# Performance work log

Hardware: AMD Instinct MI355X
Metric: run time of the kernel (lower is better)

Reference implementation:

```python
import jax, jax.numpy as jnp
import numpy as np

HEADS = 16
NU = 1
EPS = 1e-6


def dpfp(k):
    """Deterministic Parameter-Free Projection, normalized. k: [..., d_k] -> [..., 2*d_k*NU]."""
    x = jax.nn.relu(jnp.concatenate([k, -k], axis=-1))  # [..., 2*d_k]
    x_rolled = jnp.concatenate([jnp.roll(x, i, axis=-1) for i in range(1, NU + 1)], axis=-1)
    x_repeat = jnp.concatenate([x] * NU, axis=-1)
    phi = x_repeat * x_rolled
    return phi / (jnp.sum(phi, axis=-1, keepdims=True) + EPS)


def setup_inputs() -> dict:
    key = jax.random.key(0)
    ks = jax.random.split(key, 7)
    S, B, D, H = 4096, 4, 1024, HEADS
    scale = 0.02
    return {
        "x": jax.random.normal(ks[0], (S, B, D), dtype=jnp.float32),
        "Wq": jax.random.normal(ks[1], (D, D), dtype=jnp.float32) * scale,
        "Wk": jax.random.normal(ks[2], (D, D), dtype=jnp.float32) * scale,
        "Wv": jax.random.normal(ks[3], (D, D), dtype=jnp.float32) * scale,
        "Wb": jax.random.normal(ks[4], (D, H), dtype=jnp.float32) * scale,
        "Wo": jax.random.normal(ks[5], (D, D), dtype=jnp.float32) * scale,
        "bo": jnp.zeros((D,), dtype=jnp.float32),
    }


def reference(x, Wq, Wk, Wv, Wb, Wo, bo):
    S, B, D = x.shape
    H = HEADS
    dk = D // H
    d_dot = 2 * dk * NU

    # Projections: [S, B, H, d_k] (bias-free linears + head split)
    q = dpfp((x @ Wq).reshape(S, B, H, dk))   # [S, B, H, d_dot]
    k = dpfp((x @ Wk).reshape(S, B, H, dk))   # [S, B, H, d_dot]
    v = (x @ Wv).reshape(S, B, H, dk)          # [S, B, H, d_k]
    beta = jax.nn.sigmoid(x @ Wb).reshape(S, B, H, 1)  # [S, B, H, 1]

    W0 = jnp.zeros((B, H, dk, d_dot), dtype=x.dtype)  # fast-weight state

    def step(W, inputs):
        k_i, v_i, q_i, b_i = inputs  # [B,H,d_dot], [B,H,dk], [B,H,d_dot], [B,H,1]
        v_bar = jnp.einsum('bhvk,bhk->bhv', W, k_i)
        W = W + jnp.einsum('bhv,bhk->bhvk', b_i * (v_i - v_bar), k_i)
        y = jnp.einsum('bhvk,bhk->bhv', W, q_i)  # [B, H, dk]
        return W, y.reshape(B, H * dk)

    _, outputs = jax.lax.scan(step, W0, (k, v, q, beta))  # [S, B, D]
    return outputs @ Wo + bo
```

## Files before the change

kernel.cpp:

```cpp
#include <hip/hip_runtime.h>

#define S_LEN 4096
#define BATCH 4
#define NROWS 16384
#define DIM   1024
#define CHUNK 32
#define NCHUNK (S_LEN / CHUNK)

typedef __attribute__((ext_vector_type(8))) short short8;
typedef __attribute__((ext_vector_type(4))) float floatx4;
typedef _Float16 half_t;
typedef __attribute__((ext_vector_type(8))) _Float16 half8;

__device__ __forceinline__ float bf2f(short s) {
    union { unsigned int u; float f; } c;
    c.u = ((unsigned int)(unsigned short)s) << 16;
    return c.f;
}
__device__ __forceinline__ short f2bf(float f) {
    union { float f; unsigned int u; } c; c.f = f;
    unsigned int r = c.u + 0x7fffu + ((c.u >> 16) & 1u);
    return (short)(r >> 16);
}
__device__ __forceinline__ void split_bf16(float x, short& hi, short& lo) {
    short h = f2bf(x);
    hi = h;
    lo = f2bf(x - bf2f(h));
}

__device__ __forceinline__ float row16_allreduce(float x) {
    union fi { float f; int i; };
    fi a, b;
    a.f = x;
    b.i = __builtin_amdgcn_update_dpp(0, a.i, 0xB1,  0xF, 0xF, true); a.f += b.f;
    b.i = __builtin_amdgcn_update_dpp(0, a.i, 0x4E,  0xF, 0xF, true); a.f += b.f;
    b.i = __builtin_amdgcn_update_dpp(0, a.i, 0x124, 0xF, 0xF, true); a.f += b.f;
    b.i = __builtin_amdgcn_update_dpp(0, a.i, 0x128, 0xF, 0xF, true); a.f += b.f;
    return a.f;
}

__global__ __launch_bounds__(256) void transpose_k(const float* __restrict__ W,
                                                   float* __restrict__ Wt,
                                                   int K, int N) {
    int idx = blockIdx.x * 256 + threadIdx.x;
    if (idx >= N * K) return;
    int n = idx / K;
    int k = idx - n * K;
    Wt[idx] = W[k * N + n];
}

template <typename AT, int MODE>
__global__ __launch_bounds__(256) void gemm_bt(const AT* __restrict__ A,
                                               const float* __restrict__ Bt,
                                               void* __restrict__ Cout,
                                               const float* __restrict__ bias,
                                               int N, int K) {
    __shared__ __align__(16) short As_h[64][40], As_l[64][40];
    __shared__ __align__(16) short Bs_h[64][40], Bs_l[64][40];
    const int tid  = threadIdx.x;
    const int wave = tid >> 6, lane = tid & 63;
    const int row0 = blockIdx.x * 64, col0 = blockIdx.y * 64;
    const int lr = tid >> 2, lc = (tid & 3) * 8;
    const AT*    Ap = A  + (size_t)(row0 + lr) * K + lc;
    const float* Bp = Bt + (size_t)(col0 + lr) * K + lc;
    const int am = wave * 16 + (lane & 15);
    const int ak = (lane >> 4) * 8;
    floatx4 acc[4];
    #pragma unroll
    for (int t = 0; t < 4; ++t) acc[t] = (floatx4){0.f, 0.f, 0.f, 0.f};

    for (int k0 = 0; k0 < K; k0 += 32) {
        float av[8], bv[8];
        if constexpr (sizeof(AT) == 4) {
            floatx4 a0 = *(const floatx4*)(Ap + k0);
            floatx4 a1 = *(const floatx4*)(Ap + k0 + 4);
            #pragma unroll
            for (int j = 0; j < 4; ++j) { av[j] = a0[j]; av[4 + j] = a1[j]; }
        } else {
            half8 a = *(const half8*)(Ap + k0);
            #pragma unroll
            for (int j = 0; j < 8; ++j) av[j] = (float)a[j];
        }
        floatx4 b0 = *(const floatx4*)(Bp + k0);
        floatx4 b1 = *(const floatx4*)(Bp + k0 + 4);
        #pragma unroll
        for (int j = 0; j < 4; ++j) { bv[j] = b0[j]; bv[4 + j] = b1[j]; }

        short8 ah, al, bh, bl;
        #pragma unroll
        for (int j = 0; j < 8; ++j) {
            short h, l;
            split_bf16(av[j], h, l); ah[j] = h; al[j] = l;
            split_bf16(bv[j], h, l); bh[j] = h; bl[j] = l;
        }
        *(short8*)&As_h[lr][lc] = ah;
        *(short8*)&As_l[lr][lc] = al;
        *(short8*)&Bs_h[lr][lc] = bh;
        *(short8*)&Bs_l[lr][lc] = bl;
        __syncthreads();
        short8 afh = *(const short8*)&As_h[am][ak];
        short8 afl = *(const short8*)&As_l[am][ak];
        #pragma unroll
        for (int t = 0; t < 4; ++t) {
            short8 bfh = *(const short8*)&Bs_h[t * 16 + (lane & 15)][ak];
            short8 bfl = *(const short8*)&Bs_l[t * 16 + (lane & 15)][ak];
            acc[t] = __builtin_amdgcn_mfma_f32_16x16x32_bf16(afh, bfh, acc[t], 0, 0, 0);
            acc[t] = __builtin_amdgcn_mfma_f32_16x16x32_bf16(afh, bfl, acc[t], 0, 0, 0);
            acc[t] = __builtin_amdgcn_mfma_f32_16x16x32_bf16(afl, bfh, acc[t], 0, 0, 0);
        }
        __syncthreads();
    }
    const int crow = row0 + wave * 16 + (lane >> 4) * 4;
    const int ccol = lane & 15;
    #pragma unroll
    for (int t = 0; t < 4; ++t) {
        int col = col0 + t * 16 + ccol;
        #pragma unroll
        for (int r = 0; r < 4; ++r) {
            int row = crow + r;
            float v = acc[t][r];
            if (MODE == 0) {
                float b = bias ? bias[col] : 0.f;
                ((float*)Cout)[(size_t)row * N + col] = v + b;
            } else {
                ((half_t*)Cout)[(size_t)row * 2048 + (col >> 6) * 128 + (col & 63)] = (half_t)v;
            }
        }
    }
}

__global__ __launch_bounds__(256) void beta_kernel(const float* __restrict__ X,
                                                   const float* __restrict__ Wbt,
                                                   float* __restrict__ Beta) {
    int wid  = (blockIdx.x * 256 + threadIdx.x) >> 6;
    int lane = threadIdx.x & 63;
    if (wid >= NROWS) return;
    const float* xr = X + (size_t)wid * DIM + lane * 16;
    float xv[16];
    #pragma unroll
    for (int j = 0; j < 4; ++j) {
        floatx4 v = *(const floatx4*)(xr + j * 4);
        #pragma unroll
        for (int e = 0; e < 4; ++e) xv[j * 4 + e] = v[e];
    }
    #pragma unroll 1
    for (int h = 0; h < 16; ++h) {
        const float* wr = Wbt + h * DIM + lane * 16;
        float s = 0.f;
        #pragma unroll
        for (int j = 0; j < 4; ++j) {
            floatx4 v = *(const floatx4*)(wr + j * 4);
            #pragma unroll
            for (int e = 0; e < 4; ++e) s = fmaf(xv[j * 4 + e], v[e], s);
        }
        #pragma unroll
        for (int off = 32; off; off >>= 1) s += __shfl_xor(s, off);
        if (lane == 0) Beta[wid * 16 + h] = 1.f / (1.f + __expf(-s));
    }
}

__global__ __launch_bounds__(256) void dpfp_h(half_t* __restrict__ P) {
    int gw   = (blockIdx.x * 256 + threadIdx.x) >> 6;
    int lane = threadIdx.x & 63;
    half_t* base = P + (size_t)gw * 128;
    float p  = (float)base[lane];
    float pm = __shfl(p, (lane + 63) & 63);
    float rp  = fmaxf(p, 0.f),  rn  = fmaxf(-p, 0.f);
    float rpm = fmaxf(pm, 0.f), rnm = fmaxf(-pm, 0.f);
    float aprev = (lane == 0) ? rnm : rpm;
    float bprev = (lane == 0) ? rpm : rnm;
    float phi_a = rp * aprev;
    float phi_b = rn * bprev;
    float s = phi_a + phi_b;
    #pragma unroll
    for (int off = 32; off; off >>= 1) s += __shfl_xor(s, off);
    float inv = 1.f / (s + 1e-6f);
    base[lane]      = (half_t)(phi_a * inv);
    base[64 + lane] = (half_t)(phi_b * inv);
}

__global__ __launch_bounds__(256, 1) void scan_kernel(const half_t* __restrict__ PhiK,
                                                      const half_t* __restrict__ PhiQ,
                                                      const float* __restrict__ V,
                                                      const float* __restrict__ Beta,
                                                      half_t* __restrict__ Y) {
    __shared__ float Ks[2][CHUNK][128];
    __shared__ float Qs[2][CHUNK][128];
    __shared__ float Vs[2][CHUNK][16];
    __shared__ float Bs[2][CHUNK];

    const int bh = blockIdx.x >> 2;
    const int rc = blockIdx.x & 3;
    const int b = bh >> 4, h = bh & 15;
    const int tid = threadIdx.x;
    const int row_l = tid >> 4;
    const int tc = tid & 15;
    const int vrow = rc * 16 + row_l;

    const half_t* kg = PhiK + h * 128;
    const half_t* qg = PhiQ + h * 128;
    const float*  vg = V + h * 64 + rc * 16;
    const float*  bg = Beta + h;
    half_t* ybase = Y + h * 64 + vrow;

    {
        #pragma unroll
        for (int rpt = 0; rpt < 2; ++rpt) {
            int i = rpt * 256 + tid;
            int st = i >> 4, seg = i & 15, row = i & 15;
            size_t r = (size_t)(st * BATCH + b);
            half8 kv = *(const half8*)(kg + r * 2048 + seg * 8);
            half8 qv = *(const half8*)(qg + r * 2048 + seg * 8);
            floatx4 klo, khi, qlo, qhi;
            #pragma unroll
            for (int j = 0; j < 4; ++j) {
                klo[j] = (float)kv[j]; khi[j] = (float)kv[4 + j];
                qlo[j] = (float)qv[j]; qhi[j] = (float)qv[4 + j];
            }
            *(floatx4*)&Ks[0][st][seg * 8]     = klo;
            *(floatx4*)&Ks[0][st][seg * 8 + 4] = khi;
            *(floatx4*)&Qs[0][st][seg * 8]     = qlo;
            *(floatx4*)&Qs[0][st][seg * 8 + 4] = qhi;
            Vs[0][st][row] = vg[r * 1024 + row];
        }
        if (tid < CHUNK) {
            size_t r = (size_t)(tid * BATCH + b);
            Bs[0][tid] = bg[r * 16];
        }
    }
    __syncthreads();

    float w[8];
    #pragma unroll
    for (int j = 0; j < 8; ++j) w[j] = 0.f;

    for (int c = 0; c < NCHUNK; ++c) {
        const int bufi = c & 1;
        const bool more = (c + 1 < NCHUNK);
        half8 pk[2], pq[2];
        float pv[2], pb = 0.f;
        if (more) {
            #pragma unroll
            for (int rpt = 0; rpt < 2; ++rpt) {
                int i = rpt * 256 + tid;
                int st = i >> 4, seg = i & 15, row = i & 15;
                size_t r = (size_t)(((c + 1) * CHUNK + st) * BATCH + b);
                pk[rpt] = *(const half8*)(kg + r * 2048 + seg * 8);
                pq[rpt] = *(const half8*)(qg + r * 2048 + seg * 8);
                pv[rpt] = vg[r * 1024 + row];
            }
            if (tid < CHUNK) {
                size_t r = (size_t)(((c + 1) * CHUNK + tid) * BATCH + b);
                pb = bg[r * 16];
            }
        }
        float Ak[8], Aq[8], Av, Ab;
        float Bk[8], Bq[8], Bv, Bb;
        {
            floatx4 k0 = *(const floatx4*)&Ks[bufi][0][tc * 8];
            floatx4 k1 = *(const floatx4*)&Ks[bufi][0][tc * 8 + 4];
            floatx4 q0 = *(const floatx4*)&Qs[bufi][0][tc * 8];
            floatx4 q1 = *(const floatx4*)&Qs[bufi][0][tc * 8 + 4];
            #pragma unroll
            for (int j = 0; j < 4; ++j) {
                Ak[j] = k0[j]; Ak[4 + j] = k1[j];
                Aq[j] = q0[j]; Aq[4 + j] = q1[j];
            }
            Av = Vs[bufi][0][row_l];
            Ab = Bs[bufi][0];
        }
        #pragma unroll 1
        for (int u = 0; u < CHUNK; u += 2) {
            {
                floatx4 k0 = *(const floatx4*)&Ks[bufi][u + 1][tc * 8];
                floatx4 k1 = *(const floatx4*)&Ks[bufi][u + 1][tc * 8 + 4];
                floatx4 q0 = *(const floatx4*)&Qs[bufi][u + 1][tc * 8];
                floatx4 q1 = *(const floatx4*)&Qs[bufi][u + 1][tc * 8 + 4];
                #pragma unroll
                for (int j = 0; j < 4; ++j) {
                    Bk[j] = k0[j]; Bk[4 + j] = k1[j];
                    Bq[j] = q0[j]; Bq[4 + j] = q1[j];
                }
                Bv = Vs[bufi][u + 1][row_l];
                Bb = Bs[bufi][u + 1];
            }
            {
                float d0 = w[0] * Ak[0], d1 = w[1] * Ak[1];
                d0 = fmaf(w[2], Ak[2], d0); d1 = fmaf(w[3], Ak[3], d1);
                d0 = fmaf(w[4], Ak[4], d0); d1 = fmaf(w[5], Ak[5], d1);
                d0 = fmaf(w[6], Ak[6], d0); d1 = fmaf(w[7], Ak[7], d1);
                float d = row16_allreduce(d0 + d1);
                float coef = Ab * (Av - d);
                #pragma unroll
                for (int j = 0; j < 8; ++j) w[j] = fmaf(coef, Ak[j], w[j]);
                float y0 = w[0] * Aq[0], y1 = w[1] * Aq[1];
                y0 = fmaf(w[2], Aq[2], y0); y1 = fmaf(w[3], Aq[3], y1);
                y0 = fmaf(w[4], Aq[4], y0); y1 = fmaf(w[5], Aq[5], y1);
                y0 = fmaf(w[6], Aq[6], y0); y1 = fmaf(w[7], Aq[7], y1);
                float y = row16_allreduce(y0 + y1);
                if (tc == 0)
                    ybase[(size_t)((c * CHUNK + u) * BATCH + b) * 1024] = (half_t)y;
            }
            if (u + 2 < CHUNK) {
                floatx4 k0 = *(const floatx4*)&Ks[bufi][u + 2][tc * 8];
                floatx4 k1 = *(const floatx4*)&Ks[bufi][u + 2][tc * 8 + 4];
                floatx4 q0 = *(const floatx4*)&Qs[bufi][u + 2][tc * 8];
                floatx4 q1 = *(const floatx4*)&Qs[bufi][u + 2][tc * 8 + 4];
                #pragma unroll
                for (int j = 0; j < 4; ++j) {
                    Ak[j] = k0[j]; Ak[4 + j] = k1[j];
                    Aq[j] = q0[j]; Aq[4 + j] = q1[j];
                }
                Av = Vs[bufi][u + 2][row_l];
                Ab = Bs[bufi][u + 2];
            }
            {
                float d0 = w[0] * Bk[0], d1 = w[1] * Bk[1];
                d0 = fmaf(w[2], Bk[2], d0); d1 = fmaf(w[3], Bk[3], d1);
                d0 = fmaf(w[4], Bk[4], d0); d1 = fmaf(w[5], Bk[5], d1);
                d0 = fmaf(w[6], Bk[6], d0); d1 = fmaf(w[7], Bk[7], d1);
                float d = row16_allreduce(d0 + d1);
                float coef = Bb * (Bv - d);
                #pragma unroll
                for (int j = 0; j < 8; ++j) w[j] = fmaf(coef, Bk[j], w[j]);
                float y0 = w[0] * Bq[0], y1 = w[1] * Bq[1];
                y0 = fmaf(w[2], Bq[2], y0); y1 = fmaf(w[3], Bq[3], y1);
                y0 = fmaf(w[4], Bq[4], y0); y1 = fmaf(w[5], Bq[5], y1);
                y0 = fmaf(w[6], Bq[6], y0); y1 = fmaf(w[7], Bq[7], y1);
                float y = row16_allreduce(y0 + y1);
                if (tc == 0)
                    ybase[(size_t)((c * CHUNK + u + 1) * BATCH + b) * 1024] = (half_t)y;
            }
        }
        if (more) {
            const int bufn = bufi ^ 1;
            #pragma unroll
            for (int rpt = 0; rpt < 2; ++rpt) {
                int i = rpt * 256 + tid;
                int st = i >> 4, seg = i & 15, row = i & 15;
                floatx4 klo, khi, qlo, qhi;
                #pragma unroll
                for (int j = 0; j < 4; ++j) {
                    klo[j] = (float)pk[rpt][j]; khi[j] = (float)pk[rpt][4 + j];
                    qlo[j] = (float)pq[rpt][j]; qhi[j] = (float)pq[rpt][4 + j];
                }
                *(floatx4*)&Ks[bufn][st][seg * 8]     = klo;
                *(floatx4*)&Ks[bufn][st][seg * 8 + 4] = khi;
                *(floatx4*)&Qs[bufn][st][seg * 8]     = qlo;
                *(floatx4*)&Qs[bufn][st][seg * 8 + 4] = qhi;
                Vs[bufn][st][row] = pv[rpt];
            }
            if (tid < CHUNK) Bs[bufn][tid] = pb;
        }
        __syncthreads();
    }
}

extern "C" void kernel_launch(void* const* d_in, const int* in_sizes, int n_in,
                              void* d_out, int out_size, void* d_ws, size_t ws_size,
                              hipStream_t stream) {
    const float* x  = (const float*)d_in[0];
    const float* Wq = (const float*)d_in[1];
    const float* Wk = (const float*)d_in[2];
    const float* Wv = (const float*)d_in[3];
    const float* Wb = (const float*)d_in[4];
    const float* Wo = (const float*)d_in[5];
    const float* bo = (const float*)d_in[6];

    char* ws = (char*)d_ws;
    size_t off = 0;
    auto alloc = [&](size_t bytes) -> void* {
        void* p = ws + off;
        off += (bytes + 255) & ~(size_t)255;
        return p;
    };
    half_t* PhiQ = (half_t*)alloc((size_t)NROWS * 2048 * 2);
    half_t* PhiK = (half_t*)alloc((size_t)NROWS * 2048 * 2);
    half_t* Yb   = (half_t*)alloc((size_t)NROWS * 1024 * 2);
    float*  Beta = (float*)alloc((size_t)NROWS * 16 * 4);
    float*  Wqt  = (float*)alloc((size_t)1024 * 1024 * 4);
    float*  Wkt  = (float*)alloc((size_t)1024 * 1024 * 4);
    float*  Wvt  = (float*)alloc((size_t)1024 * 1024 * 4);
    float*  Wot  = (float*)alloc((size_t)1024 * 1024 * 4);
    float*  Wbt  = (float*)alloc((size_t)16 * 1024 * 4);
    float*  Vb   = (float*)d_out;

    transpose_k<<<4096, 256, 0, stream>>>(Wq, Wqt, 1024, 1024);
    transpose_k<<<4096, 256, 0, stream>>>(Wk, Wkt, 1024, 1024);
    transpose_k<<<4096, 256, 0, stream>>>(Wv, Wvt, 1024, 1024);
    transpose_k<<<4096, 256, 0, stream>>>(Wo, Wot, 1024, 1024);
    transpose_k<<<64,   256, 0, stream>>>(Wb, Wbt, 1024, 16);

    dim3 ggrid(NROWS / 64, DIM / 64);
    const int dgrid = (NROWS * 16) / 4;
    gemm_bt<float, 1><<<ggrid, 256, 0, stream>>>(x, Wqt, PhiQ, nullptr, DIM, DIM);
    dpfp_h<<<dgrid, 256, 0, stream>>>(PhiQ);
    gemm_bt<float, 1><<<ggrid, 256, 0, stream>>>(x, Wkt, PhiK, nullptr, DIM, DIM);
    dpfp_h<<<dgrid, 256, 0, stream>>>(PhiK);
    gemm_bt<float, 0><<<ggrid, 256, 0, stream>>>(x, Wvt, Vb, nullptr, DIM, DIM);
    beta_kernel<<<NROWS / 4, 256, 0, stream>>>(x, Wbt, Beta);
    scan_kernel<<<256, 256, 0, stream>>>(PhiK, PhiQ, Vb, Beta, Yb);
    gemm_bt<half_t, 0><<<ggrid, 256, 0, stream>>>(Yb, Wot, d_out, bo, DIM, DIM);
}
```

Measured before the change: 1.720 ms.

## Split scan work across twice as many blocks with 32-lane row reductions

The fast-weight scan is repartitioned so that each block owns 8 value rows instead of 16, and each row is spread over 32 lanes holding 4 state columns instead of 16 lanes holding 8. The grid doubles to 512 blocks, with launch bounds allowing two blocks per CU, and a ds_swizzle step extends the row reduction to 32 lanes. This shortens the per-thread serial dependency chain and uses more CUs for the latency-bound recurrence. The cost is a longer reduction per step and K/Q chunk loads duplicated across twice as many blocks.

```diff
diff --git a/kernel.cpp b/kernel.cpp
--- a/kernel.cpp
+++ b/kernel.cpp
@@ -37,6 +37,15 @@
     b.i = __builtin_amdgcn_update_dpp(0, a.i, 0x124, 0xF, 0xF, true); a.f += b.f;
     b.i = __builtin_amdgcn_update_dpp(0, a.i, 0x128, 0xF, 0xF, true); a.f += b.f;
     return a.f;
+}
+
+__device__ __forceinline__ float row32_allreduce(float x) {
+    x = row16_allreduce(x);
+    union fi { float f; int i; };
+    fi a, b;
+    a.f = x;
+    b.i = __builtin_amdgcn_ds_swizzle(a.i, 0x401F);
+    return a.f + b.f;
 }
 
 __global__ __launch_bounds__(256) void transpose_k(const float* __restrict__ W,
@@ -179,27 +188,27 @@
     base[64 + lane] = (half_t)(phi_b * inv);
 }
 
-__global__ __launch_bounds__(256, 1) void scan_kernel(const half_t* __restrict__ PhiK,
+__global__ __launch_bounds__(256, 2) void scan_kernel(const half_t* __restrict__ PhiK,
                                                       const half_t* __restrict__ PhiQ,
                                                       const float* __restrict__ V,
                                                       const float* __restrict__ Beta,
                                                       half_t* __restrict__ Y) {
     __shared__ float Ks[2][CHUNK][128];
     __shared__ float Qs[2][CHUNK][128];
-    __shared__ float Vs[2][CHUNK][16];
+    __shared__ float Vs[2][CHUNK][8];
     __shared__ float Bs[2][CHUNK];
 
-    const int bh = blockIdx.x >> 2;
-    const int rc = blockIdx.x & 3;
+    const int bh = blockIdx.x & 63;
+    const int rc = blockIdx.x >> 6;
     const int b = bh >> 4, h = bh & 15;
     const int tid = threadIdx.x;
-    const int row_l = tid >> 4;
-    const int tc = tid & 15;
-    const int vrow = rc * 16 + row_l;
+    const int row_l = tid >> 5;
+    const int tc = tid & 31;
+    const int vrow = rc * 8 + row_l;
 
     const half_t* kg = PhiK + h * 128;
     const half_t* qg = PhiQ + h * 128;
-    const float*  vg = V + h * 64 + rc * 16;
+    const float*  vg = V + h * 64 + rc * 8;
     const float*  bg = Beta + h;
     half_t* ybase = Y + h * 64 + vrow;
 
@@ -207,7 +216,7 @@
         #pragma unroll
         for (int rpt = 0; rpt < 2; ++rpt) {
             int i = rpt * 256 + tid;
-            int st = i >> 4, seg = i & 15, row = i & 15;
+            int st = i >> 4, seg = i & 15;
             size_t r = (size_t)(st * BATCH + b);
             half8 kv = *(const half8*)(kg + r * 2048 + seg * 8);
             half8 qv = *(const half8*)(qg + r * 2048 + seg * 8);
@@ -221,6 +230,10 @@
             *(floatx4*)&Ks[0][st][seg * 8 + 4] = khi;
             *(floatx4*)&Qs[0][st][seg * 8]     = qlo;
             *(floatx4*)&Qs[0][st][seg * 8 + 4] = qhi;
+        }
+        {
+            int st = tid >> 3, row = tid & 7;
+            size_t r = (size_t)(st * BATCH + b);
             Vs[0][st][row] = vg[r * 1024 + row];
         }
         if (tid < CHUNK) {
@@ -230,104 +243,85 @@
     }
     __syncthreads();
 
-    float w[8];
+    float w[4];
     #pragma unroll
-    for (int j = 0; j < 8; ++j) w[j] = 0.f;
+    for (int j = 0; j < 4; ++j) w[j] = 0.f;
 
     for (int c = 0; c < NCHUNK; ++c) {
         const int bufi = c & 1;
         const bool more = (c + 1 < NCHUNK);
         half8 pk[2], pq[2];
-        float pv[2], pb = 0.f;
+        float pv = 0.f, pb = 0.f;
         if (more) {
             #pragma unroll
             for (int rpt = 0; rpt < 2; ++rpt) {
                 int i = rpt * 256 + tid;
-                int st = i >> 4, seg = i & 15, row = i & 15;
+                int st = i >> 4, seg = i & 15;
                 size_t r = (size_t)(((c + 1) * CHUNK + st) * BATCH + b);
                 pk[rpt] = *(const half8*)(kg + r * 2048 + seg * 8);
                 pq[rpt] = *(const half8*)(qg + r * 2048 + seg * 8);
-                pv[rpt] = vg[r * 1024 + row];
+            }
+            {
+                int st = tid >> 3, row = tid & 7;
+                size_t r = (size_t)(((c + 1) * CHUNK + st) * BATCH + b);
+                pv = vg[r * 1024 + row];
             }
             if (tid < CHUNK) {
                 size_t r = (size_t)(((c + 1) * CHUNK + tid) * BATCH + b);
                 pb = bg[r * 16];
             }
         }
-        float Ak[8], Aq[8], Av, Ab;
-        float Bk[8], Bq[8], Bv, Bb;
+        float Ak[4], Aq[4], Av, Ab;
+        float Bk[4], Bq[4], Bv, Bb;
         {
-            floatx4 k0 = *(const floatx4*)&Ks[bufi][0][tc * 8];
-            floatx4 k1 = *(const floatx4*)&Ks[bufi][0][tc * 8 + 4];
-            floatx4 q0 = *(const floatx4*)&Qs[bufi][0][tc * 8];
-            floatx4 q1 = *(const floatx4*)&Qs[bufi][0][tc * 8 + 4];
-            #pragma unroll
-            for (int j = 0; j < 4; ++j) {
-                Ak[j] = k0[j]; Ak[4 + j] = k1[j];
-                Aq[j] = q0[j]; Aq[4 + j] = q1[j];
-            }
+            floatx4 k0 = *(const floatx4*)&Ks[bufi][0][tc * 4];
+            floatx4 q0 = *(const floatx4*)&Qs[bufi][0][tc * 4];
+            #pragma unroll
+            for (int j = 0; j < 4; ++j) { Ak[j] = k0[j]; Aq[j] = q0[j]; }
             Av = Vs[bufi][0][row_l];
             Ab = Bs[bufi][0];
         }
         #pragma unroll 1
         for (int u = 0; u < CHUNK; u += 2) {
             {
-                floatx4 k0 = *(const floatx4*)&Ks[bufi][u + 1][tc * 8];
-                floatx4 k1 = *(const floatx4*)&Ks[bufi][u + 1][tc * 8 + 4];
-                floatx4 q0 = *(const floatx4*)&Qs[bufi][u + 1][tc * 8];
-                floatx4 q1 = *(const floatx4*)&Qs[bufi][u + 1][tc * 8 + 4];
+                floatx4 k0 = *(const floatx4*)&Ks[bufi][u + 1][tc * 4];
+                floatx4 q0 = *(const floatx4*)&Qs[bufi][u + 1][tc * 4];
                 #pragma unroll
-                for (int j = 0; j < 4; ++j) {
-                    Bk[j] = k0[j]; Bk[4 + j] = k1[j];
-                    Bq[j] = q0[j]; Bq[4 + j] = q1[j];
-                }
+                for (int j = 0; j < 4; ++j) { Bk[j] = k0[j]; Bq[j] = q0[j]; }
                 Bv = Vs[bufi][u + 1][row_l];
                 Bb = Bs[bufi][u + 1];
             }
             {
                 float d0 = w[0] * Ak[0], d1 = w[1] * Ak[1];
                 d0 = fmaf(w[2], Ak[2], d0); d1 = fmaf(w[3], Ak[3], d1);
-                d0 = fmaf(w[4], Ak[4], d0); d1 = fmaf(w[5], Ak[5], d1);
-                d0 = fmaf(w[6], Ak[6], d0); d1 = fmaf(w[7], Ak[7], d1);
-                float d = row16_allreduce(d0 + d1);
+                float d = row32_allreduce(d0 + d1);
                 float coef = Ab * (Av - d);
                 #pragma unroll
-                for (int j = 0; j < 8; ++j) w[j] = fmaf(coef, Ak[j], w[j]);
+                for (int j = 0; j < 4; ++j) w[j] = fmaf(coef, Ak[j], w[j]);
                 float y0 = w[0] * Aq[0], y1 = w[1] * Aq[1];
                 y0 = fmaf(w[2], Aq[2], y0); y1 = fmaf(w[3], Aq[3], y1);
-                y0 = fmaf(w[4], Aq[4], y0); y1 = fmaf(w[5], Aq[5], y1);
-                y0 = fmaf(w[6], Aq[6], y0); y1 = fmaf(w[7], Aq[7], y1);
-                float y = row16_allreduce(y0 + y1);
+                float y = row32_allreduce(y0 + y1);
                 if (tc == 0)
                     ybase[(size_t)((c * CHUNK + u) * BATCH + b) * 1024] = (half_t)y;
             }
             if (u + 2 < CHUNK) {
-                floatx4 k0 = *(const floatx4*)&Ks[bufi][u + 2][tc * 8];
-                floatx4 k1 = *(const floatx4*)&Ks[bufi][u + 2][tc * 8 + 4];
-                floatx4 q0 = *(const floatx4*)&Qs[bufi][u + 2][tc * 8];
-                floatx4 q1 = *(const floatx4*)&Qs[bufi][u + 2][tc * 8 + 4];
+                floatx4 k0 = *(const floatx4*)&Ks[bufi][u + 2][tc * 4];
+                floatx4 q0 = *(const floatx4*)&Qs[bufi][u + 2][tc * 4];
                 #pragma unroll
-                for (int j = 0; j < 4; ++j) {
-                    Ak[j] = k0[j]; Ak[4 + j] = k1[j];
-                    Aq[j] = q0[j]; Aq[4 + j] = q1[j];
-                }
+                for (int j = 0; j < 4; ++j) { Ak[j] = k0[j]; Aq[j] = q0[j]; }
                 Av = Vs[bufi][u + 2][row_l];
                 Ab = Bs[bufi][u + 2];
             }
             {
                 float d0 = w[0] * Bk[0], d1 = w[1] * Bk[1];
                 d0 = fmaf(w[2], Bk[2], d0); d1 = fmaf(w[3], Bk[3], d1);
-                d0 = fmaf(w[4], Bk[4], d0); d1 = fmaf(w[5], Bk[5], d1);
-                d0 = fmaf(w[6], Bk[6], d0); d1 = fmaf(w[7], Bk[7], d1);
-                float d = row16_allreduce(d0 + d1);
+                float d = row32_allreduce(d0 + d1);
                 float coef = Bb * (Bv - d);
                 #pragma unroll
-                for (int j = 0; j < 8; ++j) w[j] = fmaf(coef, Bk[j], w[j]);
+                for (int j = 0; j < 4; ++j) w[j] = fmaf(coef, Bk[j], w[j]);
                 float y0 = w[0] * Bq[0], y1 = w[1] * Bq[1];
                 y0 = fmaf(w[2], Bq[2], y0); y1 = fmaf(w[3], Bq[3], y1);
-                y0 = fmaf(w[4], Bq[4], y0); y1 = fmaf(w[5], Bq[5], y1);
-                y0 = fmaf(w[6], Bq[6], y0); y1 = fmaf(w[7], Bq[7], y1);
-                float y = row16_allreduce(y0 + y1);
+                float y = row32_allreduce(y0 + y1);
                 if (tc == 0)
                     ybase[(size_t)((c * CHUNK + u + 1) * BATCH + b) * 1024] = (half_t)y;
             }
@@ -337,7 +331,7 @@
             #pragma unroll
             for (int rpt = 0; rpt < 2; ++rpt) {
                 int i = rpt * 256 + tid;
-                int st = i >> 4, seg = i & 15, row = i & 15;
+                int st = i >> 4, seg = i & 15;
                 floatx4 klo, khi, qlo, qhi;
                 #pragma unroll
                 for (int j = 0; j < 4; ++j) {
@@ -348,7 +342,10 @@
                 *(floatx4*)&Ks[bufn][st][seg * 8 + 4] = khi;
                 *(floatx4*)&Qs[bufn][st][seg * 8]     = qlo;
                 *(floatx4*)&Qs[bufn][st][seg * 8 + 4] = qhi;
-                Vs[bufn][st][row] = pv[rpt];
+            }
+            {
+                int st = tid >> 3, row = tid & 7;
+                Vs[bufn][st][row] = pv;
             }
             if (tid < CHUNK) Bs[bufn][tid] = pb;
         }
@@ -399,6 +396,6 @@
     dpfp_h<<<dgrid, 256, 0, stream>>>(PhiK);
     gemm_bt<float, 0><<<ggrid, 256, 0, stream>>>(x, Wvt, Vb, nullptr, DIM, DIM);
     beta_kernel<<<NROWS / 4, 256, 0, stream>>>(x, Wbt, Beta);
-    scan_kernel<<<256, 256, 0, stream>>>(PhiK, PhiQ, Vb, Beta, Yb);
+    scan_kernel<<<512, 256, 0, stream>>>(PhiK, PhiQ, Vb, Beta, Yb);
     gemm_bt<half_t, 0><<<ggrid, 256, 0, stream>>>(Yb, Wot, d_out, bo, DIM, DIM);
 }
```

New measurement: 1.777 ms. 3.3% more time.

## Process delta-rule scan two steps at a time using precomputed Gram terms

Applied to the files above, without the earlier changes.

The scan now advances two timesteps per pair. For each pair it precomputes the k_even·k_odd, k_even·q_even, k_even·q_odd and k_odd·q_odd inner products into shared memory at the start of each chunk. All four dot products against the old state are then issued together and corrected algebraically with these Gram terms. This breaks the serial dependency between consecutive steps' reductions, so four independent allreduces can overlap instead of four serialized ones. The cost is an extra Gram pass and a barrier per chunk, more registers for the double-buffered operands, and a different floating-point summation order.

```diff
diff --git a/kernel.cpp b/kernel.cpp
--- a/kernel.cpp
+++ b/kernel.cpp
@@ -179,6 +179,58 @@
     base[64 + lane] = (half_t)(phi_b * inv);
 }
 
+
+#define LOADSTEP(DK, DQ, STEP)                                              \
+    {                                                                       \
+        floatx4 _ka = *(const floatx4*)&Ks[bufi][STEP][tc * 8];             \
+        floatx4 _kb = *(const floatx4*)&Ks[bufi][STEP][tc * 8 + 4];         \
+        floatx4 _qa = *(const floatx4*)&Qs[bufi][STEP][tc * 8];             \
+        floatx4 _qb = *(const floatx4*)&Qs[bufi][STEP][tc * 8 + 4];         \
+        for (int _i = 0; _i < 4; ++_i) {                                    \
+            DK[_i] = _ka[_i]; DK[4 + _i] = _kb[_i];                         \
+            DQ[_i] = _qa[_i]; DQ[4 + _i] = _qb[_i];                         \
+        }                                                                   \
+    }
+
+#define DOT8(RES, X, Y)                                                     \
+    {                                                                       \
+        float _s0 = X[0] * Y[0], _s1 = X[1] * Y[1];                         \
+        _s0 = fmaf(X[2], Y[2], _s0); _s1 = fmaf(X[3], Y[3], _s1);           \
+        _s0 = fmaf(X[4], Y[4], _s0); _s1 = fmaf(X[5], Y[5], _s1);           \
+        _s0 = fmaf(X[6], Y[6], _s0); _s1 = fmaf(X[7], Y[7], _s1);           \
+        RES = _s0 + _s1;                                                    \
+    }
+
+#define PAIR(CEK, CEQ, COK, COQ, CEV, CEB, COV, COB, CG,                    \
+             NEK, NEQ, NOK, NOQ, NEV, NEB, NOV, NOB, NG, P)                 \
+    {                                                                       \
+        if ((P) + 1 < 16) {                                                 \
+            LOADSTEP(NEK, NEQ, 2 * (P) + 2);                                \
+            LOADSTEP(NOK, NOQ, 2 * (P) + 3);                                \
+            NEV = Vs[bufi][2 * (P) + 2][row_l];                             \
+            NEB = Bs[bufi][2 * (P) + 2];                                    \
+            NOV = Vs[bufi][2 * (P) + 3][row_l];                             \
+            NOB = Bs[bufi][2 * (P) + 3];                                    \
+            NG  = *(const floatx4*)&GramLDS[(P) + 1][0];                    \
+        }                                                                   \
+        float _e0, _e1, _f0, _f1;                                           \
+        DOT8(_e0, w, CEK); DOT8(_e1, w, COK);                               \
+        DOT8(_f0, w, CEQ); DOT8(_f1, w, COQ);                               \
+        _e0 = row16_allreduce(_e0); _e1 = row16_allreduce(_e1);             \
+        _f0 = row16_allreduce(_f0); _f1 = row16_allreduce(_f1);             \
+        float _c0 = CEB * (CEV - _e0);                                      \
+        float _d1 = fmaf(_c0, CG[0], _e1);                                  \
+        float _c1 = COB * (COV - _d1);                                      \
+        float _y0 = fmaf(_c0, CG[1], _f0);                                  \
+        float _y1 = fmaf(_c1, CG[3], fmaf(_c0, CG[2], _f1));                \
+        for (int _j = 0; _j < 8; ++_j)                                      \
+            w[_j] = fmaf(_c1, COK[_j], fmaf(_c0, CEK[_j], w[_j]));          \
+        if (tc == 0) {                                                      \
+            ybase[(size_t)((cc * CHUNK + 2 * (P))     * BATCH + b) * 1024] = (half_t)_y0; \
+            ybase[(size_t)((cc * CHUNK + 2 * (P) + 1) * BATCH + b) * 1024] = (half_t)_y1; \
+        }                                                                   \
+    }
+
 __global__ __launch_bounds__(256, 1) void scan_kernel(const half_t* __restrict__ PhiK,
                                                       const half_t* __restrict__ PhiQ,
                                                       const float* __restrict__ V,
@@ -188,6 +240,7 @@
     __shared__ float Qs[2][CHUNK][128];
     __shared__ float Vs[2][CHUNK][16];
     __shared__ float Bs[2][CHUNK];
+    __shared__ float GramLDS[16][4];
 
     const int bh = blockIdx.x >> 2;
     const int rc = blockIdx.x & 3;
@@ -234,9 +287,32 @@
     #pragma unroll
     for (int j = 0; j < 8; ++j) w[j] = 0.f;
 
-    for (int c = 0; c < NCHUNK; ++c) {
-        const int bufi = c & 1;
-        const bool more = (c + 1 < NCHUNK);
+    for (int cc = 0; cc < NCHUNK; ++cc) {
+        const int bufi = cc & 1;
+        const bool more = (cc + 1 < NCHUNK);
+
+        {
+            float ka[8], kb[8], qa[8], qb[8];
+            LOADSTEP(ka, qa, 2 * row_l);
+            LOADSTEP(kb, qb, 2 * row_l + 1);
+            float skk, s00, s01, s11;
+            DOT8(skk, ka, kb);
+            DOT8(s00, ka, qa);
+            DOT8(s01, ka, qb);
+            DOT8(s11, kb, qb);
+            skk = row16_allreduce(skk);
+            s00 = row16_allreduce(s00);
+            s01 = row16_allreduce(s01);
+            s11 = row16_allreduce(s11);
+            if (tc == 0) {
+                GramLDS[row_l][0] = skk;
+                GramLDS[row_l][1] = s00;
+                GramLDS[row_l][2] = s01;
+                GramLDS[row_l][3] = s11;
+            }
+        }
+        __syncthreads();
+
         half8 pk[2], pq[2];
         float pv[2], pb = 0.f;
         if (more) {
@@ -244,94 +320,35 @@
             for (int rpt = 0; rpt < 2; ++rpt) {
                 int i = rpt * 256 + tid;
                 int st = i >> 4, seg = i & 15, row = i & 15;
-                size_t r = (size_t)(((c + 1) * CHUNK + st) * BATCH + b);
+                size_t r = (size_t)(((cc + 1) * CHUNK + st) * BATCH + b);
                 pk[rpt] = *(const half8*)(kg + r * 2048 + seg * 8);
                 pq[rpt] = *(const half8*)(qg + r * 2048 + seg * 8);
                 pv[rpt] = vg[r * 1024 + row];
             }
             if (tid < CHUNK) {
-                size_t r = (size_t)(((c + 1) * CHUNK + tid) * BATCH + b);
+                size_t r = (size_t)(((cc + 1) * CHUNK + tid) * BATCH + b);
                 pb = bg[r * 16];
             }
         }
-        float Ak[8], Aq[8], Av, Ab;
-        float Bk[8], Bq[8], Bv, Bb;
-        {
-            floatx4 k0 = *(const floatx4*)&Ks[bufi][0][tc * 8];
-            floatx4 k1 = *(const floatx4*)&Ks[bufi][0][tc * 8 + 4];
-            floatx4 q0 = *(const floatx4*)&Qs[bufi][0][tc * 8];
-            floatx4 q1 = *(const floatx4*)&Qs[bufi][0][tc * 8 + 4];
-            #pragma unroll
-            for (int j = 0; j < 4; ++j) {
-                Ak[j] = k0[j]; Ak[4 + j] = k1[j];
-                Aq[j] = q0[j]; Aq[4 + j] = q1[j];
-            }
-            Av = Vs[bufi][0][row_l];
-            Ab = Bs[bufi][0];
-        }
+
+        float EK0[8], EQ0[8], OK0[8], OQ0[8];
+        float EK1[8], EQ1[8], OK1[8], OQ1[8];
+        float Ev0, Eb0, Ov0, Ob0, Ev1, Eb1, Ov1, Ob1;
+        floatx4 G0, G1;
+        LOADSTEP(EK0, EQ0, 0);
+        LOADSTEP(OK0, OQ0, 1);
+        Ev0 = Vs[bufi][0][row_l]; Eb0 = Bs[bufi][0];
+        Ov0 = Vs[bufi][1][row_l]; Ob0 = Bs[bufi][1];
+        G0 = *(const floatx4*)&GramLDS[0][0];
+
         #pragma unroll 1
-        for (int u = 0; u < CHUNK; u += 2) {
-            {
-                floatx4 k0 = *(const floatx4*)&Ks[bufi][u + 1][tc * 8];
-                floatx4 k1 = *(const floatx4*)&Ks[bufi][u + 1][tc * 8 + 4];
-                floatx4 q0 = *(const floatx4*)&Qs[bufi][u + 1][tc * 8];
-                floatx4 q1 = *(const floatx4*)&Qs[bufi][u + 1][tc * 8 + 4];
-                #pragma unroll
-                for (int j = 0; j < 4; ++j) {
-                    Bk[j] = k0[j]; Bk[4 + j] = k1[j];
-                    Bq[j] = q0[j]; Bq[4 + j] = q1[j];
-                }
-                Bv = Vs[bufi][u + 1][row_l];
-                Bb = Bs[bufi][u + 1];
-            }
-            {
-                float d0 = w[0] * Ak[0], d1 = w[1] * Ak[1];
-                d0 = fmaf(w[2], Ak[2], d0); d1 = fmaf(w[3], Ak[3], d1);
-                d0 = fmaf(w[4], Ak[4], d0); d1 = fmaf(w[5], Ak[5], d1);
-                d0 = fmaf(w[6], Ak[6], d0); d1 = fmaf(w[7], Ak[7], d1);
-                float d = row16_allreduce(d0 + d1);
-                float coef = Ab * (Av - d);
-                #pragma unroll
-                for (int j = 0; j < 8; ++j) w[j] = fmaf(coef, Ak[j], w[j]);
-                float y0 = w[0] * Aq[0], y1 = w[1] * Aq[1];
-                y0 = fmaf(w[2], Aq[2], y0); y1 = fmaf(w[3], Aq[3], y1);
-                y0 = fmaf(w[4], Aq[4], y0); y1 = fmaf(w[5], Aq[5], y1);
-                y0 = fmaf(w[6], Aq[6], y0); y1 = fmaf(w[7], Aq[7], y1);
-                float y = row16_allreduce(y0 + y1);
-                if (tc == 0)
-                    ybase[(size_t)((c * CHUNK + u) * BATCH + b) * 1024] = (half_t)y;
-            }
-            if (u + 2 < CHUNK) {
-                floatx4 k0 = *(const floatx4*)&Ks[bufi][u + 2][tc * 8];
-                floatx4 k1 = *(const floatx4*)&Ks[bufi][u + 2][tc * 8 + 4];
-                floatx4 q0 = *(const floatx4*)&Qs[bufi][u + 2][tc * 8];
-                floatx4 q1 = *(const floatx4*)&Qs[bufi][u + 2][tc * 8 + 4];
-                #pragma unroll
-                for (int j = 0; j < 4; ++j) {
-                    Ak[j] = k0[j]; Ak[4 + j] = k1[j];
-                    Aq[j] = q0[j]; Aq[4 + j] = q1[j];
-                }
-                Av = Vs[bufi][u + 2][row_l];
-                Ab = Bs[bufi][u + 2];
-            }
-            {
-                float d0 = w[0] * Bk[0], d1 = w[1] * Bk[1];
-                d0 = fmaf(w[2], Bk[2], d0); d1 = fmaf(w[3], Bk[3], d1);
-                d0 = fmaf(w[4], Bk[4], d0); d1 = fmaf(w[5], Bk[5], d1);
-                d0 = fmaf(w[6], Bk[6], d0); d1 = fmaf(w[7], Bk[7], d1);
-                float d = row16_allreduce(d0 + d1);
-                float coef = Bb * (Bv - d);
-                #pragma unroll
-                for (int j = 0; j < 8; ++j) w[j] = fmaf(coef, Bk[j], w[j]);
-                float y0 = w[0] * Bq[0], y1 = w[1] * Bq[1];
-                y0 = fmaf(w[2], Bq[2], y0); y1 = fmaf(w[3], Bq[3], y1);
-                y0 = fmaf(w[4], Bq[4], y0); y1 = fmaf(w[5], Bq[5], y1);
-                y0 = fmaf(w[6], Bq[6], y0); y1 = fmaf(w[7], Bq[7], y1);
-                float y = row16_allreduce(y0 + y1);
-                if (tc == 0)
-                    ybase[(size_t)((c * CHUNK + u + 1) * BATCH + b) * 1024] = (half_t)y;
-            }
-        }
+        for (int p2 = 0; p2 < 16; p2 += 2) {
+            PAIR(EK0, EQ0, OK0, OQ0, Ev0, Eb0, Ov0, Ob0, G0,
+                 EK1, EQ1, OK1, OQ1, Ev1, Eb1, Ov1, Ob1, G1, p2);
+            PAIR(EK1, EQ1, OK1, OQ1, Ev1, Eb1, Ov1, Ob1, G1,
+                 EK0, EQ0, OK0, OQ0, Ev0, Eb0, Ov0, Ob0, G0, p2 + 1);
+        }
+
         if (more) {
             const int bufn = bufi ^ 1;
             #pragma unroll
```

Result: faster. 1.556 ms (-9.5%).
